# Performance work log

Hardware: AMD Instinct MI355X
Metric: run time of the kernel (lower is better)

## Reference

```python
import jax, jax.numpy as jnp
import numpy as np

THRESH = 0.001
RADIUS = 0.1
NSAMPLE = 8
FRAME_DIM = 6
LOSS_WEIGHT = 1.0
EPS = 1e-7


def _ball_query(new_xyz, xyz, radius, nsample):
    # new_xyz: [N,3] query points; xyz: [F,3] candidate points
    # pointnet2 semantics: first `nsample` in-radius indices (in order),
    # remaining slots filled with the first found index (0 if none).
    d2 = jnp.sum((new_xyz[:, None, :] - xyz[None, :, :]) ** 2, axis=-1)  # [N,F]
    mask = d2 < radius * radius
    order = jnp.argsort(~mask, axis=1)[:, :nsample]          # stable: in-radius idx first
    cnt = jnp.sum(mask, axis=1)                               # [N]
    valid = jnp.arange(nsample)[None, :] < cnt[:, None]       # [N,nsample]
    return jnp.where(valid, order, order[:, :1])              # [N,nsample] int


def _face_normals(verts, faces):
    # verts: [M,3], faces: [F,3] -> unit normals [F,3]
    v = verts[faces]                                           # [F,3,3]
    n = jnp.cross(v[:, 1] - v[:, 0], v[:, 2] - v[:, 0])        # [F,3]
    norm = jnp.linalg.norm(n, axis=-1, keepdims=True)
    return n / jnp.maximum(norm, EPS)


def _contact_error_single(pred, state, h_state, h_faces):
    x_t1 = pred[:, :3]                                         # [N,3]
    x_t0 = state[:, :3]                                        # [N,3]
    h_t1 = h_state[:, :3]                                      # [M,3]
    h_t0 = h_state[:, FRAME_DIM:FRAME_DIM + 3]                 # [M,3]
    h_face_pos = jnp.mean(h_t1[h_faces], axis=-2)              # [F,3]
    h_face_prev_pos = jnp.mean(h_t0[h_faces], axis=-2)         # [F,3]
    h_face_normal = _face_normals(h_t1, h_faces)               # [F,3]
    idx = _ball_query(x_t0, h_face_prev_pos, RADIUS, NSAMPLE)  # [N,S]
    grouped_pos = h_face_pos[idx]                              # [N,S,3]
    grouped_normal = h_face_normal[idx]                        # [N,S,3]
    xyz_diff = jnp.sum((x_t1[:, None, :] - grouped_pos) * grouped_normal,
                       axis=-1, keepdims=True)                 # [N,S,1]
    interpen = jnp.maximum(THRESH - xyz_diff, 0.0)
    loss = jnp.sum(interpen ** 3, axis=-2)                     # [N,1]
    return jnp.mean(loss)                                      # reduction='mean'


def setup_inputs() -> dict:
    key = jax.random.key(0)
    k1, k2, k3, k4 = jax.random.split(key, 4)
    B, N, M, F = 2, 20000, 6890, 13776
    pred = jax.random.normal(k1, (B, N, 3), dtype=jnp.float32)
    state = jax.random.normal(k2, (B, N, 3), dtype=jnp.float32)
    h_state = jax.random.normal(k3, (B, M, 9), dtype=jnp.float32)
    h_faces = jax.random.randint(k4, (B, F, 3), 0, M, dtype=jnp.int32)
    return {"pred": pred, "state": state, "h_state": h_state, "h_faces": h_faces}


def reference(pred, state, h_state, h_faces):
    per_sample = jax.vmap(_contact_error_single)(pred, state, h_state, h_faces)  # [B]
    return jnp.mean(per_sample) * LOSS_WEIGHT
```

## Files before the change

kernel.cpp:

```cpp
#include <hip/hip_runtime.h>
#include <limits.h>

#define NB      2
#define N_Q     20000
#define NBQ     (NB * N_Q)
#define M_V     6890
#define N_F     13776
#define NBF     (NB * N_F)
#define RAD2    0.01f
#define THRESH  0.001f
#define EPSN    1e-7f
#define SCALE   (1.0f / (float)(NB * N_Q))

#define GDIM    12
#define NCELLS  (GDIM * GDIM * GDIM)
#define T_CELLS (NB * NCELLS)
#define H_INV   5.0f
#define ORG     (-1.2f)

#define QPB     8
#define QBLOCKS (NBQ / QPB)

__device__ __forceinline__ int cell_coord(float x) {
    int g = (int)floorf((x - ORG) * H_INV);
    return min(max(g, 0), GDIM - 1);
}

__device__ __forceinline__ void axis_window(float v, int& lo, int& hi) {
    float s  = (v - ORG) * H_INV;
    float fl = floorf(s);
    int g_u  = (int)fl;
    int g    = min(max(g_u, 0), GDIM - 1);
    int sy   = ((s - fl) >= 0.5f) ? 1 : -1;
    int g2   = min(max(g_u + sy, 0), GDIM - 1);
    lo = min(g, g2);
    hi = max(g, g2);
}

__device__ __forceinline__ float wave_add_f(float v) {
    #pragma unroll
    for (int m = 32; m; m >>= 1) v += __shfl_xor(v, m);
    return v;
}

__global__ __launch_bounds__(256) void face_kernel(
    const float* __restrict__ h_state,
    const int*   __restrict__ h_faces,
    float4* __restrict__ prev4,
    float4* __restrict__ pos4,
    float4* __restrict__ nrm4,
    int* __restrict__ cellid,
    int* __restrict__ cellCnt)
{
    int t = blockIdx.x * 256 + threadIdx.x;
    if (t >= NBF) return;
    int b = t / N_F;
    const int* fc = h_faces + (size_t)t * 3;
    int i0 = fc[0], i1 = fc[1], i2 = fc[2];
    const float* hs = h_state + (size_t)b * M_V * 9;

    const float* v0 = hs + (size_t)i0 * 9;
    const float* v1 = hs + (size_t)i1 * 9;
    const float* v2 = hs + (size_t)i2 * 9;

    float ax = v0[0], ay = v0[1], az = v0[2];
    float bx = v1[0], by = v1[1], bz = v1[2];
    float cx = v2[0], cy = v2[1], cz = v2[2];

    float px = (ax + bx + cx) / 3.0f;
    float py = (ay + by + cy) / 3.0f;
    float pz = (az + bz + cz) / 3.0f;

    float e1x = bx - ax, e1y = by - ay, e1z = bz - az;
    float e2x = cx - ax, e2y = cy - ay, e2z = cz - az;
    float nx = e1y * e2z - e1z * e2y;
    float ny = e1z * e2x - e1x * e2z;
    float nz = e1x * e2y - e1y * e2x;
    float nrm = sqrtf(nx * nx + ny * ny + nz * nz);
    float den = fmaxf(nrm, EPSN);
    nx /= den; ny /= den; nz /= den;

    float qx = (v0[6] + v1[6] + v2[6]) / 3.0f;
    float qy = (v0[7] + v1[7] + v2[7]) / 3.0f;
    float qz = (v0[8] + v1[8] + v2[8]) / 3.0f;

    prev4[t] = make_float4(qx, qy, qz, 0.0f);
    pos4[t]  = make_float4(px, py, pz, 0.0f);
    nrm4[t]  = make_float4(nx, ny, nz, 0.0f);

    int gx = cell_coord(qx), gy = cell_coord(qy), gz = cell_coord(qz);
    int cid = b * NCELLS + (gz * GDIM + gy) * GDIM + gx;
    cellid[t] = cid;
    atomicAdd(&cellCnt[cid], 1);
}

#define SCAN_K 14
__global__ __launch_bounds__(256) void scan_kernel(
    const int* __restrict__ cnt, int* __restrict__ start)
{
    __shared__ int sm[256];
    int t = threadIdx.x;
    int base = t * SCAN_K;
    int v[SCAN_K];
    int s = 0;
    #pragma unroll
    for (int k = 0; k < SCAN_K; ++k) {
        int idx = base + k;
        v[k] = (idx < T_CELLS) ? cnt[idx] : 0;
        s += v[k];
    }
    sm[t] = s;
    __syncthreads();
    #pragma unroll
    for (int off = 1; off < 256; off <<= 1) {
        int add = (t >= off) ? sm[t - off] : 0;
        __syncthreads();
        sm[t] += add;
        __syncthreads();
    }
    int pref = sm[t] - s;
    #pragma unroll
    for (int k = 0; k < SCAN_K; ++k) {
        int idx = base + k;
        if (idx < T_CELLS) start[idx] = pref;
        pref += v[k];
    }
    if (t == 255) start[T_CELLS] = NBF;
}

__global__ __launch_bounds__(256) void scatter_kernel(
    const int* __restrict__ cellid, int* __restrict__ cellCnt,
    const int* __restrict__ start, const float4* __restrict__ prev4,
    float4* __restrict__ prevSorted4)
{
    int t = blockIdx.x * 256 + threadIdx.x;
    if (t >= NBF) return;
    int c = cellid[t];
    int old = atomicSub(&cellCnt[c], 1);
    float4 p = prev4[t];
    p.w = __int_as_float(t);
    prevSorted4[start[c] + old - 1] = p;
}

#define CSW(a, b) { int _mn = min(a, b); int _mx = max(a, b); a = _mn; b = _mx; }

__device__ __forceinline__ int half_min_i(int v) {
    #pragma unroll
    for (int m = 16; m; m >>= 1) v = min(v, __shfl_xor(v, m));
    return v;
}

__global__ __launch_bounds__(256) void query_kernel(
    const float*  __restrict__ state,
    const float*  __restrict__ pred,
    const float4* __restrict__ prevSorted4,
    const float4* __restrict__ pos4,
    const float4* __restrict__ nrm4,
    const int* __restrict__ start,
    float* __restrict__ partials)
{
    int tid  = threadIdx.x;
    int l32  = tid & 31;
    int hw   = tid >> 5;
    int q    = blockIdx.x * QPB + hw;
    int b    = (q >= N_Q) ? 1 : 0;

    const float* st = state + (size_t)q * 3;
    float qx = st[0], qy = st[1], qz = st[2];
    const float* pr = pred + (size_t)q * 3;
    float x = pr[0], y = pr[1], z = pr[2];

    float4 P0 = pos4[b * N_F];
    float4 N0 = nrm4[b * N_F];

    int xlo, xhi, ylo, yhi, zlo, zhi;
    axis_window(qx, xlo, xhi);
    axis_window(qy, ylo, yhi);
    axis_window(qz, zlo, zhi);

    int cum1, cum2, cum3, cum4;
    int off0, off1, off2, off3;
    {
        int c0 = 0;
        #define ROW(RR, CUMP, CUMN, OFFR)                                   \
        {                                                                   \
            int gz = zlo + ((RR) >> 1), gy = ylo + ((RR) & 1);              \
            int len = 0, j0 = 0;                                            \
            if (gz <= zhi && gy <= yhi) {                                   \
                int cbase = b * NCELLS + (gz * GDIM + gy) * GDIM;           \
                j0  = start[cbase + xlo];                                   \
                len = start[cbase + xhi + 1] - j0;                          \
            }                                                               \
            OFFR = j0 - CUMP;                                               \
            CUMN = CUMP + len;                                              \
        }
        ROW(0, c0,   cum1, off0)
        ROW(1, cum1, cum2, off1)
        ROW(2, cum2, cum3, off2)
        ROW(3, cum3, cum4, off3)
        #undef ROW
    }
    int C = cum4;

    int s0 = INT_MAX, s1 = INT_MAX, s2 = INT_MAX, s3 = INT_MAX;
    int s4 = INT_MAX, s5 = INT_MAX, s6 = INT_MAX, s7 = INT_MAX;
    int cnt = 0;
    float fsum = 0.0f;
    int   lmin = INT_MAX;
    float fmin = 0.0f;

    int iters = (C + 31) >> 5;
    for (int it = 0; it < iters; ++it) {
        int k = (it << 5) + l32;
        int addr = off0 + k;
        addr = (k >= cum1) ? off1 + k : addr;
        addr = (k >= cum2) ? off2 + k : addr;
        addr = (k >= cum3) ? off3 + k : addr;
        if (k < C) {
            float4 p = prevSorted4[addr];
            float ddx = p.x - qx, ddy = p.y - qy, ddz = p.z - qz;
            float d2 = ddx * ddx + ddy * ddy + ddz * ddz;
            if (d2 < RAD2) {
                ++cnt;
                int tf = __float_as_int(p.w);
                float4 P  = pos4[tf];
                float4 Nn = nrm4[tf];
                float d = (x - P.x) * Nn.x + (y - P.y) * Nn.y + (z - P.z) * Nn.z;
                float ip = fmaxf(THRESH - d, 0.0f);
                float f = ip * ip * ip;
                fsum += f;
                if (tf < lmin) { lmin = tf; fmin = f; }
                if (tf < s7) {
                    s7 = tf;
                    CSW(s6, s7); CSW(s5, s6); CSW(s4, s5); CSW(s3, s4);
                    CSW(s2, s3); CSW(s1, s2); CSW(s0, s1);
                }
            }
        }
    }

    int   c_ = cnt;
    float fs = fsum;
    int   lm = lmin;
    float fm = fmin;
    #pragma unroll
    for (int m = 16; m; m >>= 1) {
        int   oc = __shfl_xor(c_, m);
        float os = __shfl_xor(fs, m);
        int   ol = __shfl_xor(lm, m);
        float of = __shfl_xor(fm, m);
        c_ += oc;
        fs += os;
        if (ol < lm) { lm = ol; fm = of; }
    }
    int cnt_tot = c_;

    float lsum;
    if (cnt_tot == 0) {
        float d0 = (x - P0.x) * N0.x + (y - P0.y) * N0.y + (z - P0.z) * N0.z;
        float ip0 = fmaxf(THRESH - d0, 0.0f);
        lsum = 8.0f * (ip0 * ip0 * ip0);
    } else if (cnt_tot <= 8) {
        lsum = fs + (float)(8 - cnt_tot) * fm;
    } else {
        int t0, t1, t2, t3, t4, t5, t6, t7;
#define EXTRACT(TK)                                                      \
        {                                                                \
            int m = half_min_i(s0);                                      \
            TK = m;                                                      \
            bool p = (s0 == m);                                          \
            s0 = p ? s1 : s0; s1 = p ? s2 : s1; s2 = p ? s3 : s2;        \
            s3 = p ? s4 : s3; s4 = p ? s5 : s4; s5 = p ? s6 : s5;        \
            s6 = p ? s7 : s6; s7 = p ? INT_MAX : s7;                     \
        }
        EXTRACT(t0) EXTRACT(t1) EXTRACT(t2) EXTRACT(t3)
        EXTRACT(t4) EXTRACT(t5) EXTRACT(t6) EXTRACT(t7)
#undef EXTRACT
        int v = t0;
        v = (l32 == 1) ? t1 : v;
        v = (l32 == 2) ? t2 : v;
        v = (l32 == 3) ? t3 : v;
        v = (l32 == 4) ? t4 : v;
        v = (l32 == 5) ? t5 : v;
        v = (l32 == 6) ? t6 : v;
        v = (l32 == 7) ? t7 : v;
        float4 P  = pos4[v];
        float4 Nn = nrm4[v];
        float d = (x - P.x) * Nn.x + (y - P.y) * Nn.y + (z - P.z) * Nn.z;
        float ip = fmaxf(THRESH - d, 0.0f);
        float c = ip * ip * ip;
        c = (l32 < 8) ? c : 0.0f;
        #pragma unroll
        for (int m = 16; m; m >>= 1) c += __shfl_xor(c, m);
        lsum = c;
    }

    __shared__ float ws[QPB];
    if (l32 == 0) ws[hw] = lsum;
    __syncthreads();
    if (tid == 0) {
        float s = 0.0f;
        #pragma unroll
        for (int k = 0; k < QPB; ++k) s += ws[k];
        partials[blockIdx.x] = s;
    }
}

__global__ __launch_bounds__(1024) void reduce_kernel(
    const float* __restrict__ partials, float* __restrict__ out)
{
    float s = 0.0f;
    for (int i = threadIdx.x; i < QBLOCKS; i += 1024)
        s += partials[i];
    s = wave_add_f(s);
    __shared__ float ws[16];
    int lane = threadIdx.x & 63, w = threadIdx.x >> 6;
    if (lane == 0) ws[w] = s;
    __syncthreads();
    if (threadIdx.x == 0) {
        float t = 0.0f;
        #pragma unroll
        for (int i = 0; i < 16; ++i) t += ws[i];
        out[0] = t * SCALE;
    }
}

extern "C" void kernel_launch(void* const* d_in, const int* in_sizes, int n_in,
                              void* d_out, int out_size, void* d_ws, size_t ws_size,
                              hipStream_t stream) {
    const float* pred    = (const float*)d_in[0];
    const float* state   = (const float*)d_in[1];
    const float* h_state = (const float*)d_in[2];
    const int*   h_faces = (const int*)d_in[3];
    float* out = (float*)d_out;

    float4* prev4       = (float4*)d_ws;
    float4* pos4        = prev4 + NBF;
    float4* nrm4        = pos4 + NBF;
    float4* prevSorted4 = nrm4 + NBF;
    int* cellid         = (int*)(prevSorted4 + NBF);
    int* cellCnt        = cellid + NBF;
    int* startArr       = cellCnt + T_CELLS;
    float* partials     = (float*)(startArr + T_CELLS + 1);

    hipMemsetAsync(cellCnt, 0, (size_t)T_CELLS * sizeof(int), stream);

    face_kernel<<<dim3((NBF + 255) / 256), 256, 0, stream>>>(
        h_state, h_faces, prev4, pos4, nrm4, cellid, cellCnt);

    scan_kernel<<<dim3(1), 256, 0, stream>>>(cellCnt, startArr);

    scatter_kernel<<<dim3((NBF + 255) / 256), 256, 0, stream>>>(
        cellid, cellCnt, startArr, prev4, prevSorted4);

    query_kernel<<<dim3(QBLOCKS), 256, 0, stream>>>(
        state, pred, prevSorted4, pos4, nrm4, startArr, partials);

    reduce_kernel<<<dim3(1), 1024, 0, stream>>>(partials, out);
}
```

Baseline: 48.67 us.

## Replace counting-sort grid with fixed-capacity buckets and fuse final reduction

The face kernel now writes each face's previous-frame centroid directly into a per-cell bucket of fixed capacity (CAP = 128) using the atomic slot index. This removes the single-block scan kernel, the scatter kernel and the cellid array. Face position and normal are interleaved in one array so each gather touches adjacent memory. The final reduction moves into the query kernel through a last-block-done atomic counter, which drops the separate reduce launch. In exchange, the query walks 8 individual cells instead of 4 x-rows, adding more per-iteration address selects. Faces beyond 128 in a single cell would be silently dropped, which is safe only while the cell occupancy stays below that bound.

```diff
diff --git a/kernel.cpp b/kernel.cpp
--- a/kernel.cpp
+++ b/kernel.cpp
@@ -18,6 +18,8 @@
 #define H_INV   5.0f
 #define ORG     (-1.2f)
 
+#define CAP     128
+
 #define QPB     8
 #define QBLOCKS (NBQ / QPB)
 
@@ -42,14 +44,17 @@
     for (int m = 32; m; m >>= 1) v += __shfl_xor(v, m);
     return v;
 }
+__device__ __forceinline__ int half_min_i(int v) {
+    #pragma unroll
+    for (int m = 16; m; m >>= 1) v = min(v, __shfl_xor(v, m));
+    return v;
+}
 
 __global__ __launch_bounds__(256) void face_kernel(
     const float* __restrict__ h_state,
     const int*   __restrict__ h_faces,
-    float4* __restrict__ prev4,
-    float4* __restrict__ pos4,
-    float4* __restrict__ nrm4,
-    int* __restrict__ cellid,
+    float4* __restrict__ posn,
+    float4* __restrict__ buckets,
     int* __restrict__ cellCnt)
 {
     int t = blockIdx.x * 256 + threadIdx.x;
@@ -84,81 +89,32 @@
     float qy = (v0[7] + v1[7] + v2[7]) / 3.0f;
     float qz = (v0[8] + v1[8] + v2[8]) / 3.0f;
 
-    prev4[t] = make_float4(qx, qy, qz, 0.0f);
-    pos4[t]  = make_float4(px, py, pz, 0.0f);
-    nrm4[t]  = make_float4(nx, ny, nz, 0.0f);
+    posn[2 * t]     = make_float4(px, py, pz, 0.0f);
+    posn[2 * t + 1] = make_float4(nx, ny, nz, 0.0f);
 
     int gx = cell_coord(qx), gy = cell_coord(qy), gz = cell_coord(qz);
     int cid = b * NCELLS + (gz * GDIM + gy) * GDIM + gx;
-    cellid[t] = cid;
-    atomicAdd(&cellCnt[cid], 1);
-}
-
-#define SCAN_K 14
-__global__ __launch_bounds__(256) void scan_kernel(
-    const int* __restrict__ cnt, int* __restrict__ start)
-{
-    __shared__ int sm[256];
-    int t = threadIdx.x;
-    int base = t * SCAN_K;
-    int v[SCAN_K];
-    int s = 0;
-    #pragma unroll
-    for (int k = 0; k < SCAN_K; ++k) {
-        int idx = base + k;
-        v[k] = (idx < T_CELLS) ? cnt[idx] : 0;
-        s += v[k];
-    }
-    sm[t] = s;
-    __syncthreads();
-    #pragma unroll
-    for (int off = 1; off < 256; off <<= 1) {
-        int add = (t >= off) ? sm[t - off] : 0;
-        __syncthreads();
-        sm[t] += add;
-        __syncthreads();
-    }
-    int pref = sm[t] - s;
-    #pragma unroll
-    for (int k = 0; k < SCAN_K; ++k) {
-        int idx = base + k;
-        if (idx < T_CELLS) start[idx] = pref;
-        pref += v[k];
-    }
-    if (t == 255) start[T_CELLS] = NBF;
-}
-
-__global__ __launch_bounds__(256) void scatter_kernel(
-    const int* __restrict__ cellid, int* __restrict__ cellCnt,
-    const int* __restrict__ start, const float4* __restrict__ prev4,
-    float4* __restrict__ prevSorted4)
-{
-    int t = blockIdx.x * 256 + threadIdx.x;
-    if (t >= NBF) return;
-    int c = cellid[t];
-    int old = atomicSub(&cellCnt[c], 1);
-    float4 p = prev4[t];
-    p.w = __int_as_float(t);
-    prevSorted4[start[c] + old - 1] = p;
+    int slot = atomicAdd(&cellCnt[cid], 1);
+    if (slot < CAP)
+        buckets[(size_t)cid * CAP + slot] = make_float4(qx, qy, qz, __int_as_float(t));
 }
 
 #define CSW(a, b) { int _mn = min(a, b); int _mx = max(a, b); a = _mn; b = _mx; }
-
-__device__ __forceinline__ int half_min_i(int v) {
-    #pragma unroll
-    for (int m = 16; m; m >>= 1) v = min(v, __shfl_xor(v, m));
-    return v;
-}
 
 __global__ __launch_bounds__(256) void query_kernel(
     const float*  __restrict__ state,
     const float*  __restrict__ pred,
-    const float4* __restrict__ prevSorted4,
-    const float4* __restrict__ pos4,
-    const float4* __restrict__ nrm4,
-    const int* __restrict__ start,
-    float* __restrict__ partials)
+    const float4* __restrict__ buckets,
+    const float4* __restrict__ posn,
+    const int* __restrict__ cellCnt,
+    float* __restrict__ partials,
+    int* __restrict__ doneCnt,
+    float* __restrict__ out)
 {
+    __shared__ float ws[QPB];
+    __shared__ float ws2[4];
+    __shared__ int isLast;
+
     int tid  = threadIdx.x;
     int l32  = tid & 31;
     int hw   = tid >> 5;
@@ -170,37 +126,44 @@
     const float* pr = pred + (size_t)q * 3;
     float x = pr[0], y = pr[1], z = pr[2];
 
-    float4 P0 = pos4[b * N_F];
-    float4 N0 = nrm4[b * N_F];
+    float4 P0 = posn[2 * (b * N_F)];
+    float4 N0 = posn[2 * (b * N_F) + 1];
 
     int xlo, xhi, ylo, yhi, zlo, zhi;
     axis_window(qx, xlo, xhi);
     axis_window(qy, ylo, yhi);
     axis_window(qz, zlo, zhi);
 
-    int cum1, cum2, cum3, cum4;
-    int off0, off1, off2, off3;
+    int cum1, cum2, cum3, cum4, cum5, cum6, cum7, cum8;
+    int off0, off1, off2, off3, off4, off5, off6, off7;
     {
-        int c0 = 0;
-        #define ROW(RR, CUMP, CUMN, OFFR)                                   \
+        int bN = b * NCELLS;
+        #define CELL(CI, CUMP, CUMN, OFFR)                                  \
         {                                                                   \
-            int gz = zlo + ((RR) >> 1), gy = ylo + ((RR) & 1);              \
-            int len = 0, j0 = 0;                                            \
-            if (gz <= zhi && gy <= yhi) {                                   \
-                int cbase = b * NCELLS + (gz * GDIM + gy) * GDIM;           \
-                j0  = start[cbase + xlo];                                   \
-                len = start[cbase + xhi + 1] - j0;                          \
+            int gz = zlo + ((CI) >> 2);                                     \
+            int gy = ylo + (((CI) >> 1) & 1);                               \
+            int gx = xlo + ((CI) & 1);                                      \
+            int len = 0, base = 0;                                          \
+            if (gz <= zhi && gy <= yhi && gx <= xhi) {                      \
+                int c = bN + (gz * GDIM + gy) * GDIM + gx;                  \
+                len = cellCnt[c];                                           \
+                base = c * CAP;                                             \
             }                                                               \
-            OFFR = j0 - CUMP;                                               \
+            OFFR = base - CUMP;                                             \
             CUMN = CUMP + len;                                              \
         }
-        ROW(0, c0,   cum1, off0)
-        ROW(1, cum1, cum2, off1)
-        ROW(2, cum2, cum3, off2)
-        ROW(3, cum3, cum4, off3)
-        #undef ROW
-    }
-    int C = cum4;
+        int c0 = 0;
+        CELL(0, c0,   cum1, off0)
+        CELL(1, cum1, cum2, off1)
+        CELL(2, cum2, cum3, off2)
+        CELL(3, cum3, cum4, off3)
+        CELL(4, cum4, cum5, off4)
+        CELL(5, cum5, cum6, off5)
+        CELL(6, cum6, cum7, off6)
+        CELL(7, cum7, cum8, off7)
+        #undef CELL
+    }
+    int C = cum8;
 
     int s0 = INT_MAX, s1 = INT_MAX, s2 = INT_MAX, s3 = INT_MAX;
     int s4 = INT_MAX, s5 = INT_MAX, s6 = INT_MAX, s7 = INT_MAX;
@@ -216,15 +179,19 @@
         addr = (k >= cum1) ? off1 + k : addr;
         addr = (k >= cum2) ? off2 + k : addr;
         addr = (k >= cum3) ? off3 + k : addr;
+        addr = (k >= cum4) ? off4 + k : addr;
+        addr = (k >= cum5) ? off5 + k : addr;
+        addr = (k >= cum6) ? off6 + k : addr;
+        addr = (k >= cum7) ? off7 + k : addr;
         if (k < C) {
-            float4 p = prevSorted4[addr];
+            float4 p = buckets[addr];
             float ddx = p.x - qx, ddy = p.y - qy, ddz = p.z - qz;
             float d2 = ddx * ddx + ddy * ddy + ddz * ddz;
             if (d2 < RAD2) {
                 ++cnt;
                 int tf = __float_as_int(p.w);
-                float4 P  = pos4[tf];
-                float4 Nn = nrm4[tf];
+                float4 P  = posn[2 * tf];
+                float4 Nn = posn[2 * tf + 1];
                 float d = (x - P.x) * Nn.x + (y - P.y) * Nn.y + (z - P.z) * Nn.z;
                 float ip = fmaxf(THRESH - d, 0.0f);
                 float f = ip * ip * ip;
@@ -284,8 +251,8 @@
         v = (l32 == 5) ? t5 : v;
         v = (l32 == 6) ? t6 : v;
         v = (l32 == 7) ? t7 : v;
-        float4 P  = pos4[v];
-        float4 Nn = nrm4[v];
+        float4 P  = posn[2 * v];
+        float4 Nn = posn[2 * v + 1];
         float d = (x - P.x) * Nn.x + (y - P.y) * Nn.y + (z - P.z) * Nn.z;
         float ip = fmaxf(THRESH - d, 0.0f);
         float c = ip * ip * ip;
@@ -295,33 +262,31 @@
         lsum = c;
     }
 
-    __shared__ float ws[QPB];
     if (l32 == 0) ws[hw] = lsum;
+    if (tid == 0) isLast = 0;
     __syncthreads();
+
     if (tid == 0) {
         float s = 0.0f;
         #pragma unroll
         for (int k = 0; k < QPB; ++k) s += ws[k];
         partials[blockIdx.x] = s;
-    }
-}
-
-__global__ __launch_bounds__(1024) void reduce_kernel(
-    const float* __restrict__ partials, float* __restrict__ out)
-{
-    float s = 0.0f;
-    for (int i = threadIdx.x; i < QBLOCKS; i += 1024)
-        s += partials[i];
-    s = wave_add_f(s);
-    __shared__ float ws[16];
-    int lane = threadIdx.x & 63, w = threadIdx.x >> 6;
-    if (lane == 0) ws[w] = s;
+        __threadfence();
+        int done = atomicAdd(doneCnt, 1);
+        if (done == QBLOCKS - 1) isLast = 1;
+    }
     __syncthreads();
-    if (threadIdx.x == 0) {
-        float t = 0.0f;
-        #pragma unroll
-        for (int i = 0; i < 16; ++i) t += ws[i];
-        out[0] = t * SCALE;
+
+    if (isLast) {
+        __threadfence();
+        float s = 0.0f;
+        for (int i = tid; i < QBLOCKS; i += 256)
+            s += partials[i];
+        s = wave_add_f(s);
+        if ((tid & 63) == 0) ws2[tid >> 6] = s;
+        __syncthreads();
+        if (tid == 0)
+            out[0] = (ws2[0] + ws2[1] + ws2[2] + ws2[3]) * SCALE;
     }
 }
 
@@ -334,27 +299,17 @@
     const int*   h_faces = (const int*)d_in[3];
     float* out = (float*)d_out;
 
-    float4* prev4       = (float4*)d_ws;
-    float4* pos4        = prev4 + NBF;
-    float4* nrm4        = pos4 + NBF;
-    float4* prevSorted4 = nrm4 + NBF;
-    int* cellid         = (int*)(prevSorted4 + NBF);
-    int* cellCnt        = cellid + NBF;
-    int* startArr       = cellCnt + T_CELLS;
-    float* partials     = (float*)(startArr + T_CELLS + 1);
-
-    hipMemsetAsync(cellCnt, 0, (size_t)T_CELLS * sizeof(int), stream);
+    float4* posn    = (float4*)d_ws;
+    float4* buckets = posn + 2 * NBF;
+    int* cellCnt    = (int*)(buckets + (size_t)T_CELLS * CAP);
+    int* doneCnt    = cellCnt + T_CELLS;
+    float* partials = (float*)(doneCnt + 1);
+
+    hipMemsetAsync(cellCnt, 0, (size_t)(T_CELLS + 1) * sizeof(int), stream);
 
     face_kernel<<<dim3((NBF + 255) / 256), 256, 0, stream>>>(
-        h_state, h_faces, prev4, pos4, nrm4, cellid, cellCnt);
-
-    scan_kernel<<<dim3(1), 256, 0, stream>>>(cellCnt, startArr);
-
-    scatter_kernel<<<dim3((NBF + 255) / 256), 256, 0, stream>>>(
-        cellid, cellCnt, startArr, prev4, prevSorted4);
+        h_state, h_faces, posn, buckets, cellCnt);
 
     query_kernel<<<dim3(QBLOCKS), 256, 0, stream>>>(
-        state, pred, prevSorted4, pos4, nrm4, startArr, partials);
-
-    reduce_kernel<<<dim3(1), 1024, 0, stream>>>(partials, out);
-}
+        state, pred, buckets, posn, cellCnt, partials, doneCnt, out);
+}
```

Measured after the change: 138.7 us. +184.9%, slower.
